# Optimization experiments

Hardware: AMD Instinct MI355X
Metric: run time of the kernel (lower is better)

## Reference

```python
import jax, jax.numpy as jnp
import numpy as np

N_NODES = 100000
N_EDGES = 1000000
NODE_DIM = 128
EDGE_DIM = 64
IN_DIM = 2 * NODE_DIM + EDGE_DIM  # 320


def _linear_init(key, fan_in, fan_out):
    # mimic torch nn.Linear default: U(-1/sqrt(fan_in), 1/sqrt(fan_in))
    kw, kb = jax.random.split(key)
    bound = 1.0 / np.sqrt(fan_in)
    W = jax.random.uniform(kw, (fan_in, fan_out), jnp.float32, -bound, bound)
    b = jax.random.uniform(kb, (fan_out,), jnp.float32, -bound, bound)
    return W, b


def setup_inputs() -> dict:
    key = jax.random.key(0)
    ks = jax.random.split(key, 8)
    x = jax.random.normal(ks[0], (N_NODES, NODE_DIM), jnp.float32)
    edge_index = jax.random.randint(ks[1], (2, N_EDGES), 0, N_NODES, jnp.int64 if jax.config.read('jax_enable_x64') else jnp.int32)
    edge_features = jax.random.normal(ks[2], (N_EDGES, EDGE_DIM), jnp.float32)
    W1, b1 = _linear_init(ks[3], IN_DIM, 256)
    W2, b2 = _linear_init(ks[4], 256, 128)
    W3, b3 = _linear_init(ks[5], 128, 64)
    W4, b4 = _linear_init(ks[6], 64, 1)
    return {
        'x': x, 'edge_index': edge_index, 'edge_features': edge_features,
        'num_nodes': N_NODES,
        'W1': W1, 'b1': b1, 'W2': W2, 'b2': b2,
        'W3': W3, 'b3': b3, 'W4': W4, 'b4': b4,
    }


def reference(x, edge_index, edge_features, num_nodes, W1, b1, W2, b2, W3, b3, W4, b4):
    v = edge_index[0]
    u = edge_index[1]
    # gather endpoint embeddings and concat with edge features: [E, 2*node_dim+edge_dim]
    pair = jnp.concatenate([x[v], x[u], edge_features], axis=-1)
    h = jax.nn.relu(pair @ W1 + b1)
    h = jax.nn.relu(h @ W2 + b2)
    h = jax.nn.relu(h @ W3 + b3)
    pred = h @ W4 + b4  # [E, 1]
    return pred
```

## Files before the change

kernel.cpp:

```cpp
#include <hip/hip_runtime.h>
#include <hip/hip_bf16.h>

typedef __bf16 bf16;
typedef __attribute__((ext_vector_type(8))) __bf16 bf16x8;
typedef __attribute__((ext_vector_type(4))) __bf16 bf16x4;
typedef __attribute__((ext_vector_type(4))) float f32x4;

#define E_TOTAL   1000000
#define NODE_DIM  128
#define EDGE_DIM  64

#define SA_STRIDE  328
#define SH1_STRIDE 264
#define SH2_STRIDE 136

#define SMEM_BYTES 52224
#define SH2_OFF    33792
#define SP_OFF     51200

#define WS_XBF_BYTES 25600000
#define WB_W2F  163840
#define WB_W3F  (163840 + 65536)
#define WB_CANO (163840 + 65536 + 16384)
#define WB_FLAG (163840 + 65536 + 16384 + 2064)
#define WB_END  (163840 + 65536 + 16384 + 2064 + 16)
#define WS_NEED (WS_XBF_BYTES + WB_END)

__device__ inline int plausible16(const unsigned short* h) {
    int c = 0;
    for (int i = 0; i < 64; ++i) {
        int e = (h[i] >> 7) & 0xFF;
        if (e >= 90 && e <= 151) ++c;
    }
    return c;
}

__global__ void sniff(const void* x, const void* ei, const void* ef,
                      const void* W1, int* flags) {
    if (threadIdx.x == 0 && blockIdx.x == 0) {
        flags[0] = (plausible16((const unsigned short*)x)  < 52) ? 1 : 0;
        flags[1] = (plausible16((const unsigned short*)ef) < 52) ? 1 : 0;
        flags[2] = (plausible16((const unsigned short*)W1) < 52) ? 1 : 0;
        const int* w = (const int*)ei;
        int oz = 0, lo_ok = 1;
        for (int i = 1; i < 32; i += 2) if (w[i] == 0) ++oz;
        for (int i = 0; i < 32; i += 2) if ((unsigned)w[i] >= 100000u) lo_ok = 0;
        flags[3] = (oz == 16 && lo_ok) ? 1 : 0;
    }
}

__device__ inline float loadF(const void* p, int isf, int i) {
    return isf ? ((const float*)p)[i] : (float)((const bf16*)p)[i];
}

__global__ void canonicalize(const void* W1, const void* W2, const void* W3,
                             const void* b1, const void* b2, const void* b3,
                             const void* W4, const void* b4,
                             bf16* W1f, bf16* W2f, bf16* W3f,
                             float* cano, const int* flags) {
    int isf = flags[2];
    int o = blockIdx.x * 256 + threadIdx.x;
    if (o < 81920) {
        int jj = o & 7, lane = (o >> 3) & 63, t2 = o >> 9;
        int ks = t2 % 10, jt = t2 / 10;
        int k = ks * 32 + (lane >> 4) * 8 + jj;
        int n = jt * 16 + (lane & 15);
        W1f[o] = (bf16)loadF(W1, isf, k * 256 + n);
    } else if (o < 114688) {
        int o2 = o - 81920;
        int jj = o2 & 7, lane = (o2 >> 3) & 63, t2 = o2 >> 9;
        int ks = t2 & 7, jt = t2 >> 3;
        int k = ks * 32 + (lane >> 4) * 8 + jj;
        int n = jt * 16 + (lane & 15);
        W2f[o2] = (bf16)loadF(W2, isf, k * 128 + n);
    } else if (o < 122880) {
        int o3 = o - 114688;
        int jj = o3 & 7, lane = (o3 >> 3) & 63, t2 = o3 >> 9;
        int ks = t2 & 3, jt = t2 >> 2;
        int k = ks * 32 + (lane >> 4) * 8 + jj;
        int n = jt * 16 + (lane & 15);
        W3f[o3] = (bf16)loadF(W3, isf, k * 64 + n);
    } else if (o < 123396) {
        int j = o - 122880;
        float v;
        if (j < 256)       v = loadF(b1, isf, j);
        else if (j < 384)  v = loadF(b2, isf, j - 256);
        else if (j < 448)  v = loadF(b3, isf, j - 384);
        else if (j == 448) v = loadF(b4, isf, 0);
        else if (j < 452)  v = 0.f;
        else               v = loadF(W4, isf, j - 452);
        cano[j] = v;
    }
}

__global__ void convert_x(const void* x, bf16* xbf, const int* flags) {
    int i = (blockIdx.x * 256 + threadIdx.x) * 4;
    if (flags[0]) {
        const float* f = (const float*)x + i;
        bf16 v0 = (bf16)f[0], v1 = (bf16)f[1], v2 = (bf16)f[2], v3 = (bf16)f[3];
        xbf[i] = v0; xbf[i + 1] = v1; xbf[i + 2] = v2; xbf[i + 3] = v3;
    } else {
        *(unsigned long long*)(xbf + i) = *(const unsigned long long*)((const bf16*)x + i);
    }
}

__global__ __launch_bounds__(256, 3) void fused_mlp(
    const void* __restrict__ xs, const int* __restrict__ ei, const void* __restrict__ ef,
    const bf16* __restrict__ W1f, const bf16* __restrict__ W2f,
    const bf16* __restrict__ W3f,
    const float* __restrict__ cano, const int* __restrict__ flags,
    int xmode_host, float* __restrict__ out)
{
    __shared__ __align__(16) char smem[SMEM_BYTES];
    bf16*  sA  = (bf16*)smem;
    bf16*  sH1 = (bf16*)smem;
    bf16*  sH2 = (bf16*)(smem + SH2_OFF);
    float* sP  = (float*)(smem + SP_OFF);

    const int tid  = threadIdx.x;
    const int wave = tid >> 6;
    const int lane = tid & 63;
    const int quad = lane >> 4;
    const int l16  = lane & 15;
    const int e0   = blockIdx.x * 64;

    const int isfe = flags[1];
    const int is64 = flags[3];
    const int xm   = (xmode_host < 0) ? flags[0] : xmode_host;

    const bf16* w1base = W1f + (size_t)wave * (40 * 512) + lane * 8;
    const bf16* w2base = W2f + (size_t)wave * (16 * 512) + lane * 8;
    const bf16* w3base = W3f + (size_t)wave * (4 * 512) + lane * 8;

    {
        const int xrow0 = tid >> 5;
        const int xseg  = tid & 31;
        const int which = xseg >> 4;
        const int xk    = (xseg & 15) << 3;
        if (xm == 0) {
            const bf16* xsb = (const bf16*)xs;
            bf16x8 xb[8];
#pragma unroll
            for (int i = 0; i < 8; ++i) {
                int row = i * 8 + xrow0;
                size_t pos = which ? (size_t)(E_TOTAL + e0 + row) : (size_t)(e0 + row);
                int node = is64 ? ei[2 * pos] : ei[pos];
                xb[i] = *(const bf16x8*)(xsb + (size_t)node * NODE_DIM + xk);
            }
#pragma unroll
            for (int i = 0; i < 8; ++i)
                *(bf16x8*)&sA[(i * 8 + xrow0) * SA_STRIDE + xseg * 8] = xb[i];
        } else {
            const float* xsf = (const float*)xs;
            float xf[8][8];
#pragma unroll
            for (int i = 0; i < 8; ++i) {
                int row = i * 8 + xrow0;
                size_t pos = which ? (size_t)(E_TOTAL + e0 + row) : (size_t)(e0 + row);
                int node = is64 ? ei[2 * pos] : ei[pos];
                const float* f = xsf + (size_t)node * NODE_DIM + xk;
#pragma unroll
                for (int j = 0; j < 8; ++j) xf[i][j] = f[j];
            }
#pragma unroll
            for (int i = 0; i < 8; ++i) {
                bf16x8 v;
#pragma unroll
                for (int j = 0; j < 8; ++j) v[j] = (bf16)xf[i][j];
                *(bf16x8*)&sA[(i * 8 + xrow0) * SA_STRIDE + xseg * 8] = v;
            }
        }
        int seg = tid & 7, r0 = tid >> 3, r1 = r0 + 32;
        int kst = 256 + seg * 8;
        if (isfe) {
            const float* f0 = (const float*)ef + (size_t)(e0 + r0) * EDGE_DIM + seg * 8;
            const float* f1 = (const float*)ef + (size_t)(e0 + r1) * EDGE_DIM + seg * 8;
            float a0[8], a1[8];
#pragma unroll
            for (int j = 0; j < 8; ++j) { a0[j] = f0[j]; a1[j] = f1[j]; }
            bf16x8 v0, v1;
#pragma unroll
            for (int j = 0; j < 8; ++j) { v0[j] = (bf16)a0[j]; v1[j] = (bf16)a1[j]; }
            *(bf16x8*)&sA[r0 * SA_STRIDE + kst] = v0;
            *(bf16x8*)&sA[r1 * SA_STRIDE + kst] = v1;
        } else {
            const bf16* eb = (const bf16*)ef;
            bf16x8 v0 = *(const bf16x8*)(eb + (size_t)(e0 + r0) * EDGE_DIM + seg * 8);
            bf16x8 v1 = *(const bf16x8*)(eb + (size_t)(e0 + r1) * EDGE_DIM + seg * 8);
            *(bf16x8*)&sA[r0 * SA_STRIDE + kst] = v0;
            *(bf16x8*)&sA[r1 * SA_STRIDE + kst] = v1;
        }
    }
    bf16x8 w1pre[4];
#pragma unroll
    for (int p = 0; p < 4; ++p)
        w1pre[p] = *(const bf16x8*)(w1base + (p * 10 + 0) * 512);
    __syncthreads();

    f32x4 acc1[4][4];
#pragma unroll
    for (int p = 0; p < 4; ++p)
#pragma unroll
        for (int q = 0; q < 4; ++q)
            acc1[p][q] = (f32x4){0.f, 0.f, 0.f, 0.f};

#pragma unroll
    for (int ks = 0; ks < 10; ++ks) {
        bf16x8 w[4], e[4];
#pragma unroll
        for (int p = 0; p < 4; ++p)
            w[p] = (ks == 0) ? w1pre[p]
                             : *(const bf16x8*)(w1base + (p * 10 + ks) * 512);
#pragma unroll
        for (int q = 0; q < 4; ++q)
            e[q] = *(const bf16x8*)&sA[(16 * q + l16) * SA_STRIDE + ks * 32 + quad * 8];
        __builtin_amdgcn_s_setprio(1);
#pragma unroll
        for (int p = 0; p < 4; ++p)
#pragma unroll
            for (int q = 0; q < 4; ++q)
                acc1[p][q] = __builtin_amdgcn_mfma_f32_16x16x32_bf16(
                    w[p], e[q], acc1[p][q], 0, 0, 0);
        __builtin_amdgcn_s_setprio(0);
    }
    __syncthreads();
    {
#pragma unroll
        for (int p = 0; p < 4; ++p) {
            f32x4 bias = *(const f32x4*)&cano[64 * wave + 16 * p + 4 * quad];
#pragma unroll
            for (int q = 0; q < 4; ++q) {
                bf16x4 pv;
#pragma unroll
                for (int r = 0; r < 4; ++r)
                    pv[r] = (bf16)fmaxf(acc1[p][q][r] + bias[r], 0.f);
                *(bf16x4*)&sH1[(16 * q + l16) * SH1_STRIDE + 64 * wave + 16 * p + 4 * quad] = pv;
            }
        }
    }
    bf16x8 w2pre[2];
#pragma unroll
    for (int p = 0; p < 2; ++p)
        w2pre[p] = *(const bf16x8*)(w2base + (p * 8 + 0) * 512);
    __syncthreads();

    f32x4 acc2[2][4];
#pragma unroll
    for (int p = 0; p < 2; ++p)
#pragma unroll
        for (int q = 0; q < 4; ++q)
            acc2[p][q] = (f32x4){0.f, 0.f, 0.f, 0.f};
#pragma unroll
    for (int ks = 0; ks < 8; ++ks) {
        bf16x8 w[2], e[4];
#pragma unroll
        for (int p = 0; p < 2; ++p)
            w[p] = (ks == 0) ? w2pre[p]
                             : *(const bf16x8*)(w2base + (p * 8 + ks) * 512);
#pragma unroll
        for (int q = 0; q < 4; ++q)
            e[q] = *(const bf16x8*)&sH1[(16 * q + l16) * SH1_STRIDE + ks * 32 + quad * 8];
        __builtin_amdgcn_s_setprio(1);
#pragma unroll
        for (int p = 0; p < 2; ++p)
#pragma unroll
            for (int q = 0; q < 4; ++q)
                acc2[p][q] = __builtin_amdgcn_mfma_f32_16x16x32_bf16(
                    w[p], e[q], acc2[p][q], 0, 0, 0);
        __builtin_amdgcn_s_setprio(0);
    }
    {
#pragma unroll
        for (int p = 0; p < 2; ++p) {
            f32x4 bias = *(const f32x4*)&cano[256 + 32 * wave + 16 * p + 4 * quad];
#pragma unroll
            for (int q = 0; q < 4; ++q) {
                bf16x4 pv;
#pragma unroll
                for (int r = 0; r < 4; ++r)
                    pv[r] = (bf16)fmaxf(acc2[p][q][r] + bias[r], 0.f);
                *(bf16x4*)&sH2[(16 * q + l16) * SH2_STRIDE + 32 * wave + 16 * p + 4 * quad] = pv;
            }
        }
    }
    bf16x8 w3pre = *(const bf16x8*)(w3base + 0 * 512);
    __syncthreads();

    f32x4 acc3[4];
#pragma unroll
    for (int q = 0; q < 4; ++q) acc3[q] = (f32x4){0.f, 0.f, 0.f, 0.f};
#pragma unroll
    for (int ks = 0; ks < 4; ++ks) {
        bf16x8 w = (ks == 0) ? w3pre : *(const bf16x8*)(w3base + ks * 512);
        bf16x8 e[4];
#pragma unroll
        for (int q = 0; q < 4; ++q)
            e[q] = *(const bf16x8*)&sH2[(16 * q + l16) * SH2_STRIDE + ks * 32 + quad * 8];
        __builtin_amdgcn_s_setprio(1);
#pragma unroll
        for (int q = 0; q < 4; ++q)
            acc3[q] = __builtin_amdgcn_mfma_f32_16x16x32_bf16(w, e[q], acc3[q], 0, 0, 0);
        __builtin_amdgcn_s_setprio(0);
    }

    {
        f32x4 b3v = *(const f32x4*)&cano[384 + 16 * wave + 4 * quad];
        f32x4 w4v = *(const f32x4*)&cano[452 + 16 * wave + 4 * quad];
        float pq[4];
#pragma unroll
        for (int q = 0; q < 4; ++q) {
            float s = 0.f;
#pragma unroll
            for (int r = 0; r < 4; ++r)
                s += fmaxf(acc3[q][r] + b3v[r], 0.f) * w4v[r];
            s += __shfl_xor(s, 16);
            s += __shfl_xor(s, 32);
            pq[q] = s;
        }
        float mine = (quad == 0) ? pq[0] : (quad == 1) ? pq[1]
                   : (quad == 2) ? pq[2] : pq[3];
        sP[(16 * quad + l16) * 4 + wave] = mine;
    }
    __syncthreads();

    if (tid < 64) {
        f32x4 v = *(const f32x4*)&sP[tid * 4];
        out[e0 + tid] = v[0] + v[1] + v[2] + v[3] + cano[448];
    }
}

extern "C" void kernel_launch(void* const* d_in, const int* in_sizes, int n_in,
                              void* d_out, int out_size, void* d_ws, size_t ws_size,
                              hipStream_t stream) {
    const void* x  = d_in[0];
    const int*  ei = (const int*)d_in[1];
    const void* ef = d_in[2];
    const void* W1 = d_in[4];
    const void* b1 = d_in[5];
    const void* W2 = d_in[6];
    const void* b2 = d_in[7];
    const void* W3 = d_in[8];
    const void* b3 = d_in[9];
    const void* W4 = d_in[10];
    const void* b4 = d_in[11];
    float* out = (float*)d_out;

    char* ws = (char*)d_ws;
    const bool big = ws_size >= (size_t)WS_NEED;
    bf16* xbf   = (bf16*)ws;
    char* wbase = big ? (ws + WS_XBF_BYTES) : ws;
    bf16*  W1f   = (bf16*)wbase;
    bf16*  W2f   = (bf16*)(wbase + WB_W2F);
    bf16*  W3f   = (bf16*)(wbase + WB_W3F);
    float* cano  = (float*)(wbase + WB_CANO);
    int*   flags = (int*)(wbase + WB_FLAG);

    sniff<<<1, 64, 0, stream>>>(x, ei, ef, W1, flags);
    canonicalize<<<483, 256, 0, stream>>>(W1, W2, W3, b1, b2, b3, W4, b4,
                                          W1f, W2f, W3f, cano, flags);
    if (big) convert_x<<<12500, 256, 0, stream>>>(x, xbf, flags);
    fused_mlp<<<E_TOTAL / 64, 256, 0, stream>>>(
        big ? (const void*)xbf : x, ei, ef, W1f, W2f, W3f,
        cano, flags, big ? 0 : -1, out);
}
```

Before: 612.5 us.

## Inline dtype sniffing per wave, vectorize x conversion, prefetch more weights

Removes the single-thread sniff kernel and its flags buffer. Each wave now detects the input dtype and index width with a ballot over the first elements, which saves one launch and a serialized tiny kernel. convert_x handles 8 elements per thread with vector loads and stores. The fused MLP prefetches more weight fragments ahead of each layer's MFMA loop (two k-steps for layer 1, all of W2 and W3) to hide global latency, at the cost of higher register pressure that may reduce occupancy.

After: 599.4 us. 2.1% less time.

```diff
diff --git a/kernel.cpp b/kernel.cpp
--- a/kernel.cpp
+++ b/kernel.cpp
@@ -22,31 +22,24 @@
 #define WB_W2F  163840
 #define WB_W3F  (163840 + 65536)
 #define WB_CANO (163840 + 65536 + 16384)
-#define WB_FLAG (163840 + 65536 + 16384 + 2064)
 #define WB_END  (163840 + 65536 + 16384 + 2064 + 16)
 #define WS_NEED (WS_XBF_BYTES + WB_END)
 
-__device__ inline int plausible16(const unsigned short* h) {
-    int c = 0;
-    for (int i = 0; i < 64; ++i) {
-        int e = (h[i] >> 7) & 0xFF;
-        if (e >= 90 && e <= 151) ++c;
-    }
-    return c;
-}
-
-__global__ void sniff(const void* x, const void* ei, const void* ef,
-                      const void* W1, int* flags) {
-    if (threadIdx.x == 0 && blockIdx.x == 0) {
-        flags[0] = (plausible16((const unsigned short*)x)  < 52) ? 1 : 0;
-        flags[1] = (plausible16((const unsigned short*)ef) < 52) ? 1 : 0;
-        flags[2] = (plausible16((const unsigned short*)W1) < 52) ? 1 : 0;
-        const int* w = (const int*)ei;
-        int oz = 0, lo_ok = 1;
-        for (int i = 1; i < 32; i += 2) if (w[i] == 0) ++oz;
-        for (int i = 0; i < 32; i += 2) if ((unsigned)w[i] >= 100000u) lo_ok = 0;
-        flags[3] = (oz == 16 && lo_ok) ? 1 : 0;
-    }
+__device__ inline int wave_is_f32(const void* p, int lane) {
+    unsigned short h = ((const unsigned short*)p)[lane];
+    int e = (h >> 7) & 0xFF;
+    unsigned long long b = __ballot(e >= 90 && e <= 151);
+    return (__popcll(b) < 52) ? 1 : 0;
+}
+
+__device__ inline int wave_is_i64(const int* ei, int lane) {
+    int ok = 1;
+    if (lane < 32) {
+        int v = ei[lane];
+        ok = (lane & 1) ? (v == 0) : ((unsigned)v < 100000u);
+    }
+    unsigned long long b = __ballot(ok);
+    return (b == ~0ull) ? 1 : 0;
 }
 
 __device__ inline float loadF(const void* p, int isf, int i) {
@@ -56,9 +49,8 @@
 __global__ void canonicalize(const void* W1, const void* W2, const void* W3,
                              const void* b1, const void* b2, const void* b3,
                              const void* W4, const void* b4,
-                             bf16* W1f, bf16* W2f, bf16* W3f,
-                             float* cano, const int* flags) {
-    int isf = flags[2];
+                             bf16* W1f, bf16* W2f, bf16* W3f, float* cano) {
+    int isf = wave_is_f32(W1, threadIdx.x & 63);
     int o = blockIdx.x * 256 + threadIdx.x;
     if (o < 81920) {
         int jj = o & 7, lane = (o >> 3) & 63, t2 = o >> 9;
@@ -93,14 +85,19 @@
     }
 }
 
-__global__ void convert_x(const void* x, bf16* xbf, const int* flags) {
-    int i = (blockIdx.x * 256 + threadIdx.x) * 4;
-    if (flags[0]) {
+__global__ void convert_x(const void* x, bf16* xbf) {
+    int isf = wave_is_f32(x, threadIdx.x & 63);
+    size_t i = ((size_t)blockIdx.x * 256 + threadIdx.x) * 8;
+    if (isf) {
         const float* f = (const float*)x + i;
-        bf16 v0 = (bf16)f[0], v1 = (bf16)f[1], v2 = (bf16)f[2], v3 = (bf16)f[3];
-        xbf[i] = v0; xbf[i + 1] = v1; xbf[i + 2] = v2; xbf[i + 3] = v3;
+        f32x4 a = *(const f32x4*)f;
+        f32x4 c = *(const f32x4*)(f + 4);
+        bf16x8 v;
+#pragma unroll
+        for (int j = 0; j < 4; ++j) { v[j] = (bf16)a[j]; v[j + 4] = (bf16)c[j]; }
+        *(bf16x8*)(xbf + i) = v;
     } else {
-        *(unsigned long long*)(xbf + i) = *(const unsigned long long*)((const bf16*)x + i);
+        *(bf16x8*)(xbf + i) = *(const bf16x8*)((const bf16*)x + i);
     }
 }
 
@@ -108,7 +105,7 @@
     const void* __restrict__ xs, const int* __restrict__ ei, const void* __restrict__ ef,
     const bf16* __restrict__ W1f, const bf16* __restrict__ W2f,
     const bf16* __restrict__ W3f,
-    const float* __restrict__ cano, const int* __restrict__ flags,
+    const float* __restrict__ cano,
     int xmode_host, float* __restrict__ out)
 {
     __shared__ __align__(16) char smem[SMEM_BYTES];
@@ -124,9 +121,9 @@
     const int l16  = lane & 15;
     const int e0   = blockIdx.x * 64;
 
-    const int isfe = flags[1];
-    const int is64 = flags[3];
-    const int xm   = (xmode_host < 0) ? flags[0] : xmode_host;
+    const int isfe = wave_is_f32(ef, lane);
+    const int is64 = wave_is_i64(ei, lane);
+    const int xm   = (xmode_host >= 0) ? xmode_host : wave_is_f32(xs, lane);
 
     const bf16* w1base = W1f + (size_t)wave * (40 * 512) + lane * 8;
     const bf16* w2base = W2f + (size_t)wave * (16 * 512) + lane * 8;
@@ -191,10 +188,12 @@
             *(bf16x8*)&sA[r1 * SA_STRIDE + kst] = v1;
         }
     }
-    bf16x8 w1pre[4];
-#pragma unroll
-    for (int p = 0; p < 4; ++p)
-        w1pre[p] = *(const bf16x8*)(w1base + (p * 10 + 0) * 512);
+    bf16x8 w1pre[2][4];
+#pragma unroll
+    for (int ks = 0; ks < 2; ++ks)
+#pragma unroll
+        for (int p = 0; p < 4; ++p)
+            w1pre[ks][p] = *(const bf16x8*)(w1base + (p * 10 + ks) * 512);
     __syncthreads();
 
     f32x4 acc1[4][4];
@@ -209,8 +208,8 @@
         bf16x8 w[4], e[4];
 #pragma unroll
         for (int p = 0; p < 4; ++p)
-            w[p] = (ks == 0) ? w1pre[p]
-                             : *(const bf16x8*)(w1base + (p * 10 + ks) * 512);
+            w[p] = (ks < 2) ? w1pre[ks][p]
+                            : *(const bf16x8*)(w1base + (p * 10 + ks) * 512);
 #pragma unroll
         for (int q = 0; q < 4; ++q)
             e[q] = *(const bf16x8*)&sA[(16 * q + l16) * SA_STRIDE + ks * 32 + quad * 8];
@@ -224,6 +223,12 @@
         __builtin_amdgcn_s_setprio(0);
     }
     __syncthreads();
+    bf16x8 w2pre[2][8];
+#pragma unroll
+    for (int p = 0; p < 2; ++p)
+#pragma unroll
+        for (int ks = 0; ks < 8; ++ks)
+            w2pre[p][ks] = *(const bf16x8*)(w2base + (p * 8 + ks) * 512);
     {
 #pragma unroll
         for (int p = 0; p < 4; ++p) {
@@ -238,25 +243,17 @@
             }
         }
     }
-    bf16x8 w2pre[2];
+    __syncthreads();
+
+    f32x4 acc2[2][4];
 #pragma unroll
     for (int p = 0; p < 2; ++p)
-        w2pre[p] = *(const bf16x8*)(w2base + (p * 8 + 0) * 512);
-    __syncthreads();
-
-    f32x4 acc2[2][4];
-#pragma unroll
-    for (int p = 0; p < 2; ++p)
 #pragma unroll
         for (int q = 0; q < 4; ++q)
             acc2[p][q] = (f32x4){0.f, 0.f, 0.f, 0.f};
 #pragma unroll
     for (int ks = 0; ks < 8; ++ks) {
-        bf16x8 w[2], e[4];
-#pragma unroll
-        for (int p = 0; p < 2; ++p)
-            w[p] = (ks == 0) ? w2pre[p]
-                             : *(const bf16x8*)(w2base + (p * 8 + ks) * 512);
+        bf16x8 e[4];
 #pragma unroll
         for (int q = 0; q < 4; ++q)
             e[q] = *(const bf16x8*)&sH1[(16 * q + l16) * SH1_STRIDE + ks * 32 + quad * 8];
@@ -266,9 +263,13 @@
 #pragma unroll
             for (int q = 0; q < 4; ++q)
                 acc2[p][q] = __builtin_amdgcn_mfma_f32_16x16x32_bf16(
-                    w[p], e[q], acc2[p][q], 0, 0, 0);
+                    w2pre[p][ks], e[q], acc2[p][q], 0, 0, 0);
         __builtin_amdgcn_s_setprio(0);
     }
+    bf16x8 w3pre[4];
+#pragma unroll
+    for (int ks = 0; ks < 4; ++ks)
+        w3pre[ks] = *(const bf16x8*)(w3base + ks * 512);
     {
 #pragma unroll
         for (int p = 0; p < 2; ++p) {
@@ -283,7 +284,6 @@
             }
         }
     }
-    bf16x8 w3pre = *(const bf16x8*)(w3base + 0 * 512);
     __syncthreads();
 
     f32x4 acc3[4];
@@ -291,7 +291,6 @@
     for (int q = 0; q < 4; ++q) acc3[q] = (f32x4){0.f, 0.f, 0.f, 0.f};
 #pragma unroll
     for (int ks = 0; ks < 4; ++ks) {
-        bf16x8 w = (ks == 0) ? w3pre : *(const bf16x8*)(w3base + ks * 512);
         bf16x8 e[4];
 #pragma unroll
         for (int q = 0; q < 4; ++q)
@@ -299,7 +298,7 @@
         __builtin_amdgcn_s_setprio(1);
 #pragma unroll
         for (int q = 0; q < 4; ++q)
-            acc3[q] = __builtin_amdgcn_mfma_f32_16x16x32_bf16(w, e[q], acc3[q], 0, 0, 0);
+            acc3[q] = __builtin_amdgcn_mfma_f32_16x16x32_bf16(w3pre[ks], e[q], acc3[q], 0, 0, 0);
         __builtin_amdgcn_s_setprio(0);
     }
 
@@ -353,13 +352,11 @@
     bf16*  W2f   = (bf16*)(wbase + WB_W2F);
     bf16*  W3f   = (bf16*)(wbase + WB_W3F);
     float* cano  = (float*)(wbase + WB_CANO);
-    int*   flags = (int*)(wbase + WB_FLAG);
-
-    sniff<<<1, 64, 0, stream>>>(x, ei, ef, W1, flags);
+
     canonicalize<<<483, 256, 0, stream>>>(W1, W2, W3, b1, b2, b3, W4, b4,
-                                          W1f, W2f, W3f, cano, flags);
-    if (big) convert_x<<<12500, 256, 0, stream>>>(x, xbf, flags);
+                                          W1f, W2f, W3f, cano);
+    if (big) convert_x<<<6250, 256, 0, stream>>>(x, xbf);
     fused_mlp<<<E_TOTAL / 64, 256, 0, stream>>>(
         big ? (const void*)xbf : x, ei, ef, W1f, W2f, W3f,
-        cano, flags, big ? 0 : -1, out);
-}
+        cano, big ? 0 : -1, out);
+}
```
